# Performance work log

Hardware: AMD Instinct MI355X
Metric: run time of the kernel (lower is better)

Reference implementation:

```python
import jax, jax.numpy as jnp
import numpy as np

B, L, C, H, W = 2, 16, 16, 64, 64


def setup_inputs() -> dict:
    key = jax.random.key(0)
    k1, k2 = jax.random.split(key)
    # flows scaled so cumulative normalized-coordinate flows mostly stay in [-1, 1]
    flows = jax.random.normal(k1, (B, L, 2, H, W), dtype=jnp.float32) * 0.05
    images = jax.random.normal(k2, (B, L, C, H, W), dtype=jnp.float32)
    return {"flows": flows, "images": images}


def _bilinear_sample(images, gx, gy):
    # images: [B, Lj, C, H, W]; gx, gy: [B, Li, Lj, H, W] normalized coords in [-1, 1]
    # Replicates torch.nn.functional.grid_sample(mode='bilinear',
    # padding_mode='zeros', align_corners=False).
    Bs, Lj, Cs, Hs, Ws = images.shape
    ix = ((gx + 1.0) * Ws - 1.0) * 0.5  # pixel x coord
    iy = ((gy + 1.0) * Hs - 1.0) * 0.5  # pixel y coord
    x0f = jnp.floor(ix)
    y0f = jnp.floor(iy)
    wx = ix - x0f  # weight toward x0+1 (differentiable w.r.t. flow)
    wy = iy - y0f
    x0 = x0f.astype(jnp.int32)
    y0 = y0f.astype(jnp.int32)
    img_flat = images.reshape(Bs, Lj, Cs, Hs * Ws)

    def gather(xi, yi):
        valid = (xi >= 0) & (xi < Ws) & (yi >= 0) & (yi < Hs)  # [B,Li,Lj,H,W]
        lin = jnp.clip(yi, 0, Hs - 1) * Ws + jnp.clip(xi, 0, Ws - 1)
        lin_t = jnp.transpose(lin, (0, 2, 1, 3, 4))  # [B,Lj,Li,H,W]
        # per (b, j): gather [C, HW] at indices [Li, H, W] -> [C, Li, H, W]
        v = jax.vmap(jax.vmap(lambda im, l: im[:, l]))(img_flat, lin_t)
        v = jnp.transpose(v, (0, 3, 1, 2, 4, 5))  # [B,Li,Lj,C,H,W]
        return v * valid[:, :, :, None, :, :].astype(v.dtype)

    v00 = gather(x0, y0)
    v01 = gather(x0 + 1, y0)
    v10 = gather(x0, y0 + 1)
    v11 = gather(x0 + 1, y0 + 1)
    wX = wx[:, :, :, None, :, :]
    wY = wy[:, :, :, None, :, :]
    return (v00 * (1.0 - wX) * (1.0 - wY) + v01 * wX * (1.0 - wY)
            + v10 * (1.0 - wX) * wY + v11 * wX * wY)


def reference(flows, images):
    Bs, Ls, _, Hs, Ws = flows.shape
    dt = flows.dtype
    cum = jnp.cumsum(flows, axis=1)  # [B,L,2,H,W]
    # rel[b, i, j] = cum[b, i] - cum[b, j]  -> [B,Li,Lj,2,H,W]
    rel = cum[:, :, None] - cum[:, None, :]
    # base sampling grid (pixel centers in normalized coords)
    gx_base = (jnp.arange(Ws, dtype=dt) + 0.5) * (2.0 / Ws) - 1.0  # [W]
    gy_base = (jnp.arange(Hs, dtype=dt) + 0.5) * (2.0 / Hs) - 1.0  # [H]
    gx = gx_base + rel[:, :, :, 0]              # [B,Li,Lj,H,W]
    gy = gy_base[:, None] + rel[:, :, :, 1]     # [B,Li,Lj,H,W]
    gx = jnp.remainder(gx + 1.0, 2.0) - 1.0     # wrap x into [-1, 1)
    warped = _bilinear_sample(images, gx, gy)   # [B,Li,Lj,C,H,W]
    mask = jnp.tril(jnp.ones((Ls, Ls), dtype=dt))
    # causal accumulate over source index j
    return jnp.einsum('bijchw,ij->bichw', warped, mask)
```

## Files before the change

### kernel.cpp

```cpp
#include <hip/hip_runtime.h>

#define BB 2
#define LL 16
#define CC 16
#define HH 64
#define WW 64
#define HWSZ (HH * WW)
#define NSEG 36

__device__ __constant__ int SEG_I[NSEG] = {
    1, 2, 3, 4,
    5, 5, 6, 6, 7, 7, 8, 8,
    9, 9, 9, 10, 10, 10, 11, 11, 11, 12, 12, 12,
    13, 13, 13, 13, 14, 14, 14, 14, 15, 15, 15, 15};
__device__ __constant__ int SEG_J0[NSEG] = {
    0, 0, 0, 0,
    0, 4, 0, 4, 0, 4, 0, 4,
    0, 4, 8, 0, 4, 8, 0, 4, 8, 0, 4, 8,
    0, 4, 8, 12, 0, 4, 8, 12, 0, 4, 8, 12};

#define CUM2_FLOATS (BB * LL * HWSZ * 2)

__global__ __launch_bounds__(256) void gsp_prep(
    const float* __restrict__ flows,
    const float* __restrict__ images,
    float2* __restrict__ cum2,
    float4* __restrict__ nhwc,
    float* __restrict__ out)
{
    if (blockIdx.x < 32) {
        const int gid = blockIdx.x * 256 + threadIdx.x;
        const int b   = gid >> 12;
        const int pix = gid & (HWSZ - 1);
        const float* fb = flows + (size_t)b * LL * 2 * HWSZ + pix;
        float vx[LL], vy[LL];
        #pragma unroll
        for (int l = 0; l < LL; ++l) {
            vx[l] = fb[(size_t)l * 2 * HWSZ];
            vy[l] = fb[(size_t)l * 2 * HWSZ + HWSZ];
        }
        #pragma unroll
        for (int l = 1; l < LL; ++l) { vx[l] += vx[l - 1]; vy[l] += vy[l - 1]; }
        float2* cb = cum2 + (size_t)b * LL * HWSZ + pix;
        #pragma unroll
        for (int l = 0; l < LL; ++l) {
            float2 v; v.x = vx[l]; v.y = vy[l];
            cb[(size_t)l * HWSZ] = v;
        }
    } else {
        const int gid  = (blockIdx.x - 32) * 256 + threadIdx.x;
        const int quad = gid & 3;
        const int pix  = (gid >> 2) & (HWSZ - 1);
        const int bl   = gid >> 14;

        const float* src = images + (size_t)(bl * CC + quad * 4) * HWSZ + pix;
        float4 v;
        v.x = src[0 * HWSZ];
        v.y = src[1 * HWSZ];
        v.z = src[2 * HWSZ];
        v.w = src[3 * HWSZ];
        nhwc[(size_t)(bl * HWSZ + pix) * 4 + quad] = v;

        float* op = out + (size_t)(bl * CC + quad * 4) * HWSZ + pix;
        op[0 * HWSZ] = v.x;
        op[1 * HWSZ] = v.y;
        op[2 * HWSZ] = v.z;
        op[3 * HWSZ] = v.w;
    }
}

__global__ __launch_bounds__(256) void gsp_pairs(
    const float2* __restrict__ cum2,
    const float4* __restrict__ nhwc,
    float* __restrict__ out)
{
    const int tile = blockIdx.x & 63;
    const int seg  = (blockIdx.x >> 6) % NSEG;
    const int b    = blockIdx.x / (64 * NSEG);

    const int i    = SEG_I[seg];
    const int j0   = SEG_J0[seg];
    const int jmax = i - 1;

    const int psub = threadIdx.x >> 2;
    const int quad = threadIdx.x & 3;
    const int pix  = tile * 64 + psub;
    const int h = pix >> 6;
    const int w = pix & (WW - 1);

    const float2* cum_b  = cum2 + (size_t)b * LL * HWSZ + pix;
    const float4* nhwc_b = nhwc + (size_t)b * LL * HWSZ * 4;

    const float gxb = (w + 0.5f) * (2.0f / WW) - 1.0f;
    const float gyb = (h + 0.5f) * (2.0f / HH) - 1.0f;

    const float2 ci = cum_b[(size_t)i * HWSZ];
    int   jj[4];
    float2 cj[4];
    #pragma unroll
    for (int k = 0; k < 4; ++k) {
        jj[k] = min(j0 + k, jmax);
        cj[k] = cum_b[(size_t)jj[k] * HWSZ];
    }

    int   off[16];
    float fxk[4], fyk[4];
    float m00[4], m01[4], m10[4], m11[4];
    #pragma unroll
    for (int k = 0; k < 4; ++k) {
        float gx = gxb + (ci.x - cj[k].x);
        float gy = gyb + (ci.y - cj[k].y);

        float tt = gx + 1.0f;
        tt = tt - floorf(tt * 0.5f) * 2.0f;
        gx = tt - 1.0f;

        const float ix = ((gx + 1.0f) * WW - 1.0f) * 0.5f;
        const float iy = ((gy + 1.0f) * HH - 1.0f) * 0.5f;
        const float x0f = floorf(ix);
        const float y0f = floorf(iy);
        fxk[k] = ix - x0f;
        fyk[k] = iy - y0f;
        const int x0 = (int)x0f;
        const int y0 = (int)y0f;
        const int x1 = x0 + 1;
        const int y1 = y0 + 1;

        const bool vx0 = (x0 >= 0) && (x0 < WW);
        const bool vx1 = (x1 >= 0) && (x1 < WW);
        const bool vy0 = (y0 >= 0) && (y0 < HH);
        const bool vy1 = (y1 >= 0) && (y1 < HH);
        const float wpad = (j0 + k <= jmax) ? 1.0f : 0.0f;
        m00[k] = (vx0 && vy0) ? wpad : 0.0f;
        m01[k] = (vx1 && vy0) ? wpad : 0.0f;
        m10[k] = (vx0 && vy1) ? wpad : 0.0f;
        m11[k] = (vx1 && vy1) ? wpad : 0.0f;

        const int cx0 = min(max(x0, 0), WW - 1);
        const int cx1 = min(max(x1, 0), WW - 1);
        const int cy0 = min(max(y0, 0), HH - 1);
        const int cy1 = min(max(y1, 0), HH - 1);

        const int jbase = jj[k] * (HWSZ * 4) + quad;
        off[k * 4 + 0] = jbase + (cy0 * WW + cx0) * 4;
        off[k * 4 + 1] = jbase + (cy0 * WW + cx1) * 4;
        off[k * 4 + 2] = jbase + (cy1 * WW + cx0) * 4;
        off[k * 4 + 3] = jbase + (cy1 * WW + cx1) * 4;
    }

    float4 v[16];
    #pragma unroll
    for (int m = 0; m < 16; ++m) v[m] = nhwc_b[off[m]];

    float wgt[16];
    #pragma unroll
    for (int k = 0; k < 4; ++k) {
        const float fx = fxk[k], fy = fyk[k];
        wgt[k * 4 + 0] = m00[k] * (1.0f - fx) * (1.0f - fy);
        wgt[k * 4 + 1] = m01[k] * fx * (1.0f - fy);
        wgt[k * 4 + 2] = m10[k] * (1.0f - fx) * fy;
        wgt[k * 4 + 3] = m11[k] * fx * fy;
    }

    float ax = 0.0f, ay = 0.0f, az = 0.0f, aw = 0.0f;
    #pragma unroll
    for (int m = 0; m < 16; ++m) {
        ax += wgt[m] * v[m].x;
        ay += wgt[m] * v[m].y;
        az += wgt[m] * v[m].z;
        aw += wgt[m] * v[m].w;
    }

    float* op = out + ((size_t)(b * LL + i) * CC + quad * 4) * HWSZ + pix;
    atomicAdd(op + 0 * HWSZ, ax);
    atomicAdd(op + 1 * HWSZ, ay);
    atomicAdd(op + 2 * HWSZ, az);
    atomicAdd(op + 3 * HWSZ, aw);
}

extern "C" void kernel_launch(void* const* d_in, const int* in_sizes, int n_in,
                              void* d_out, int out_size, void* d_ws, size_t ws_size,
                              hipStream_t stream) {
    const float* flows  = (const float*)d_in[0];
    const float* images = (const float*)d_in[1];
    float* out = (float*)d_out;
    float2* cum2 = (float2*)d_ws;
    float*  nhwc = (float*)d_ws + CUM2_FLOATS;

    gsp_prep<<<32 + 2048, 256, 0, stream>>>(flows, images, cum2, (float4*)nhwc, out);

    const int grid = BB * NSEG * 64;
    gsp_pairs<<<grid, 256, 0, stream>>>(cum2, (const float4*)nhwc, out);
}
```

Before: 91.62 us.

## Replace atomic accumulation with per-segment partials and a deterministic reduce kernel

The pairs kernel now writes each segment's 4-channel sum into a partial buffer instead of issuing four scattered atomicAdds to the output. A new reduce kernel adds the identity image term and the partials for each output frame, then writes the output. This removes atomic contention and the prep kernel's copy of images into the output, at the cost of an extra launch and extra global traffic through the partial buffer (36 segments × 2 batches × 16 channels × HW floats).

Result: no change. 89.89 us (-1.9%).

```diff
diff --git a/kernel.cpp b/kernel.cpp
--- a/kernel.cpp
+++ b/kernel.cpp
@@ -19,14 +19,22 @@
     0, 4, 8, 0, 4, 8, 0, 4, 8, 0, 4, 8,
     0, 4, 8, 12, 0, 4, 8, 12, 0, 4, 8, 12};
 
+__device__ __constant__ signed char NSEG_OF_I[LL] = {0,1,1,1,1,2,2,2,2,3,3,3,3,4,4,4};
+__device__ __constant__ signed char SEG_OF_I[LL][4] = {
+    {0,0,0,0},
+    {0,0,0,0}, {1,0,0,0}, {2,0,0,0}, {3,0,0,0},
+    {4,5,0,0}, {6,7,0,0}, {8,9,0,0}, {10,11,0,0},
+    {12,13,14,0}, {15,16,17,0}, {18,19,20,0}, {21,22,23,0},
+    {24,25,26,27}, {28,29,30,31}, {32,33,34,35}};
+
 #define CUM2_FLOATS (BB * LL * HWSZ * 2)
+#define QP_FLOATS   (BB * LL * CC * HWSZ)
 
 __global__ __launch_bounds__(256) void gsp_prep(
     const float* __restrict__ flows,
     const float* __restrict__ images,
     float2* __restrict__ cum2,
-    float4* __restrict__ nhwc,
-    float* __restrict__ out)
+    float4* __restrict__ nhwc)
 {
     if (blockIdx.x < 32) {
         const int gid = blockIdx.x * 256 + threadIdx.x;
@@ -59,20 +67,14 @@
         v.y = src[1 * HWSZ];
         v.z = src[2 * HWSZ];
         v.w = src[3 * HWSZ];
-        nhwc[(size_t)(bl * HWSZ + pix) * 4 + quad] = v;
-
-        float* op = out + (size_t)(bl * CC + quad * 4) * HWSZ + pix;
-        op[0 * HWSZ] = v.x;
-        op[1 * HWSZ] = v.y;
-        op[2 * HWSZ] = v.z;
-        op[3 * HWSZ] = v.w;
+        nhwc[((size_t)bl * HWSZ + pix) * 4 + quad] = v;
     }
 }
 
 __global__ __launch_bounds__(256) void gsp_pairs(
     const float2* __restrict__ cum2,
     const float4* __restrict__ nhwc,
-    float* __restrict__ out)
+    float4* __restrict__ partial)
 {
     const int tile = blockIdx.x & 63;
     const int seg  = (blockIdx.x >> 6) % NSEG;
@@ -95,7 +97,7 @@
     const float gyb = (h + 0.5f) * (2.0f / HH) - 1.0f;
 
     const float2 ci = cum_b[(size_t)i * HWSZ];
-    int   jj[4];
+    int    jj[4];
     float2 cj[4];
     #pragma unroll
     for (int k = 0; k < 4; ++k) {
@@ -162,20 +164,43 @@
         wgt[k * 4 + 3] = m11[k] * fx * fy;
     }
 
-    float ax = 0.0f, ay = 0.0f, az = 0.0f, aw = 0.0f;
+    float4 s; s.x = 0.0f; s.y = 0.0f; s.z = 0.0f; s.w = 0.0f;
     #pragma unroll
     for (int m = 0; m < 16; ++m) {
-        ax += wgt[m] * v[m].x;
-        ay += wgt[m] * v[m].y;
-        az += wgt[m] * v[m].z;
-        aw += wgt[m] * v[m].w;
-    }
-
-    float* op = out + ((size_t)(b * LL + i) * CC + quad * 4) * HWSZ + pix;
-    atomicAdd(op + 0 * HWSZ, ax);
-    atomicAdd(op + 1 * HWSZ, ay);
-    atomicAdd(op + 2 * HWSZ, az);
-    atomicAdd(op + 3 * HWSZ, aw);
+        s.x += wgt[m] * v[m].x;
+        s.y += wgt[m] * v[m].y;
+        s.z += wgt[m] * v[m].z;
+        s.w += wgt[m] * v[m].w;
+    }
+    partial[((size_t)(b * NSEG + seg) * HWSZ + pix) * 4 + quad] = s;
+}
+
+__global__ __launch_bounds__(256) void gsp_reduce(
+    const float4* __restrict__ nhwc,
+    const float4* __restrict__ partial,
+    float* __restrict__ out)
+{
+    const int gid  = blockIdx.x * 256 + threadIdx.x;
+    const int quad = gid & 3;
+    const int pix  = (gid >> 2) & (HWSZ - 1);
+    const int bl   = gid >> 14;
+    const int b    = bl >> 4;
+    const int i    = bl & 15;
+
+    float4 s = nhwc[((size_t)bl * HWSZ + pix) * 4 + quad];
+
+    const int n = NSEG_OF_I[i];
+    for (int k = 0; k < n; ++k) {
+        const int seg = SEG_OF_I[i][k];
+        const float4 p = partial[((size_t)(b * NSEG + seg) * HWSZ + pix) * 4 + quad];
+        s.x += p.x; s.y += p.y; s.z += p.z; s.w += p.w;
+    }
+
+    float* op = out + ((size_t)bl * CC + quad * 4) * HWSZ + pix;
+    op[0 * HWSZ] = s.x;
+    op[1 * HWSZ] = s.y;
+    op[2 * HWSZ] = s.z;
+    op[3 * HWSZ] = s.w;
 }
 
 extern "C" void kernel_launch(void* const* d_in, const int* in_sizes, int n_in,
@@ -184,11 +209,14 @@
     const float* flows  = (const float*)d_in[0];
     const float* images = (const float*)d_in[1];
     float* out = (float*)d_out;
-    float2* cum2 = (float2*)d_ws;
-    float*  nhwc = (float*)d_ws + CUM2_FLOATS;
-
-    gsp_prep<<<32 + 2048, 256, 0, stream>>>(flows, images, cum2, (float4*)nhwc, out);
+    float2* cum2    = (float2*)d_ws;
+    float*  nhwc    = (float*)d_ws + CUM2_FLOATS;
+    float4* partial = (float4*)((float*)d_ws + CUM2_FLOATS + QP_FLOATS);
+
+    gsp_prep<<<32 + 2048, 256, 0, stream>>>(flows, images, cum2, (float4*)nhwc);
 
     const int grid = BB * NSEG * 64;
-    gsp_pairs<<<grid, 256, 0, stream>>>(cum2, (const float4*)nhwc, out);
-}
+    gsp_pairs<<<grid, 256, 0, stream>>>(cum2, (const float4*)nhwc, partial);
+
+    gsp_reduce<<<2048, 256, 0, stream>>>((const float4*)nhwc, partial, out);
+}
```
